# Kernel optimization log

Hardware: AMD Instinct MI355X
Metric: run time of the kernel (lower is better)

## Reference

```python
import jax, jax.numpy as jnp
import numpy as np

N = 4096
IN, HID, OUT = 512, 512, 512
EMB, MHID = 64, 128
GRID_SIZE, SPLINE_ORDER = 5, 3
D_B = GRID_SIZE + SPLINE_ORDER + 1      # 9
SPLINE_DIM = GRID_SIZE + SPLINE_ORDER   # 8


def make_grid():
    h = (1.0 - (-1.0)) / GRID_SIZE
    return jnp.arange(-SPLINE_ORDER, GRID_SIZE + SPLINE_ORDER + 1, dtype=jnp.float32) * h - 1.0


def b_splines(x, grid):
    # x: (N, in) -> (N, in, SPLINE_DIM); Cox-de Boor recursion, epsilon-stabilized
    xg = x[..., None]
    bases = ((xg >= grid[:-1]) & (xg < grid[1:])).astype(x.dtype)
    eps = 1e-08
    for k in range(1, SPLINE_ORDER + 1):
        dp = grid[k:-1] - grid[:-(k + 1)]
        dn = grid[k + 1:] - grid[1:-k]
        bases = (xg - grid[:-(k + 1)]) / (dp + eps) * bases[..., :-1] \
              + (grid[k + 1:] - xg) / (dn + eps) * bases[..., 1:]
    return bases


def _xavier(k, shape):
    fan_out, fan_in = shape
    std = (2.0 / (fan_in + fan_out)) ** 0.5
    return std * jax.random.normal(k, shape, jnp.float32)


def setup_inputs() -> dict:
    key = jax.random.key(0)
    ks = jax.random.split(key, 7)
    x = 2.0 * jax.random.uniform(ks[0], (N, IN), jnp.float32) - 1.0
    inp = {"x": x}
    dims = [(IN, HID), (HID, OUT)]
    for i, (fi, fo) in enumerate(dims):
        kk = jax.random.split(ks[i + 1], 3)
        inp[f"emb{i}"] = _xavier(kk[0], (fi * fo, EMB))   # layout: (out, in) flattened, out outer
        inp[f"w1_{i}"] = _xavier(kk[1], (MHID, EMB))
        inp[f"b1_{i}"] = jnp.zeros((MHID,), jnp.float32)
        inp[f"w2_{i}"] = _xavier(kk[2], (D_B, MHID))
        inp[f"b2_{i}"] = jnp.zeros((D_B,), jnp.float32)
    return inp


def _kan_layer(h, emb, w1, b1, w2, b2, in_f, out_f, grid):
    basis = b_splines(h, grid)                              # (N, in, SPLINE_DIM)
    w = (emb @ w1.T + b1) @ w2.T + b2                       # (out*in, D_B)
    w = w.reshape(out_f, in_f, D_B)
    w_spline = w[..., :SPLINE_DIM]                          # (out, in, SPLINE_DIM)
    w_base = w[..., SPLINE_DIM]                             # (out, in)  == weights[:, :, -1]
    out = jnp.einsum('nis,ois->no', basis, w_spline)
    out = out + jnp.einsum('ni,oi->no', jax.nn.silu(h), w_base)
    return out


def reference(x, emb0, w1_0, b1_0, w2_0, b2_0, emb1, w1_1, b1_1, w2_1, b2_1):
    grid = make_grid()
    h = _kan_layer(x, emb0, w1_0, b1_0, w2_0, b2_0, IN, HID, grid)
    h = _kan_layer(h, emb1, w1_1, b1_1, w2_1, b2_1, HID, OUT, grid)
    return h
```

## Files before the change

kernel.cpp:

```cpp
#include <hip/hip_runtime.h>
#include <cstdint>
#include <cstddef>

typedef unsigned short u16;
typedef unsigned int   u32;

typedef __bf16 bf16x8 __attribute__((ext_vector_type(8)));
typedef float  f32x4  __attribute__((ext_vector_type(4)));

#define NROWS 4096
#define INF   512
#define OUTF  512
#define EMB   64
#define MHID  128
#define DB    9
#define KDIM  (INF * DB)
#define MN    (NROWS * OUTF)

__device__ __forceinline__ u16 f2bf(float f) {
    union { float f; u32 ui; } v; v.f = f;
    u32 u = v.ui;
    u += 0x7fffu + ((u >> 16) & 1u);
    return (u16)(u >> 16);
}
__device__ __forceinline__ float gridv(int t) { return (float)(t - 3) * 0.4f - 1.0f; }

__global__ __launch_bounds__(256) void meff_kernel(
    const float* __restrict__ w1_0, const float* __restrict__ b1_0,
    const float* __restrict__ w2_0, const float* __restrict__ b2_0,
    const float* __restrict__ w1_1, const float* __restrict__ b1_1,
    const float* __restrict__ w2_1, const float* __restrict__ b2_1,
    float* __restrict__ Mc)
{
    int tid  = threadIdx.x;
    int lane = tid & 63;
    int wid  = blockIdx.x * 4 + (tid >> 6);
    if (wid >= 1170) return;
    int layer = wid / 585;
    int o     = wid % 585;
    const float* w1 = layer ? w1_1 : w1_0;
    const float* b1 = layer ? b1_1 : b1_0;
    const float* w2 = layer ? w2_1 : w2_0;
    const float* b2 = layer ? b2_1 : b2_0;

    float p;
    int d;
    if (o < 576) {
        int j = o / 9; d = o % 9;
        p = w1[lane * EMB + j]        * w2[d * MHID + lane]
          + w1[(lane + 64) * EMB + j] * w2[d * MHID + lane + 64];
    } else {
        d = o - 576;
        p = b1[lane] * w2[d * MHID + lane] + b1[lane + 64] * w2[d * MHID + lane + 64];
    }
#pragma unroll
    for (int off = 32; off >= 1; off >>= 1)
        p += __shfl_xor(p, off, 64);
    if (lane == 0) {
        if (o >= 576) p += b2[d];
        Mc[layer * 1024 + o] = p;
    }
}

__global__ __launch_bounds__(256) void genw_kernel(
    const float* __restrict__ emb0, const float* __restrict__ emb1,
    const float* __restrict__ Mc,
    u16* __restrict__ Bw0, u16* __restrict__ Bw1)
{
    __shared__ __align__(16) float tile[256 * 65];
    __shared__ float Ms[64 * 12];
    __shared__ float Cs[9];

    int layer = blockIdx.y;
    const float* emb = layer ? emb1 : emb0;
    u16* Bw = layer ? Bw1 : Bw0;
    const float* mc = Mc + layer * 1024;

    int tid = threadIdx.x;
    for (int idx = tid; idx < 585; idx += 256) {
        float v = mc[idx];
        if (idx < 576) Ms[(idx / 9) * 12 + (idx % 9)] = v;
        else Cs[idx - 576] = v;
    }

    size_t rowbase = (size_t)blockIdx.x * 256;
    const float4* g4 = (const float4*)(emb + rowbase * EMB);
#pragma unroll
    for (int it = 0; it < 16; ++it) {
        int f = it * 256 + tid;
        float4 v = g4[f];
        int row = f >> 4, c4 = (f & 15) * 4;
        float* t = &tile[row * 65 + c4];
        t[0] = v.x; t[1] = v.y; t[2] = v.z; t[3] = v.w;
    }
    __syncthreads();

    float acc[9];
#pragma unroll
    for (int d = 0; d < 9; ++d) acc[d] = Cs[d];

    const float* myrow = &tile[tid * 65];
#pragma unroll
    for (int jj = 0; jj < 16; ++jj) {
        float v0 = myrow[jj * 4 + 0];
        float v1 = myrow[jj * 4 + 1];
        float v2 = myrow[jj * 4 + 2];
        float v3 = myrow[jj * 4 + 3];
        const float* m0 = &Ms[(jj * 4 + 0) * 12];
        const float* m1 = &Ms[(jj * 4 + 1) * 12];
        const float* m2 = &Ms[(jj * 4 + 2) * 12];
        const float* m3 = &Ms[(jj * 4 + 3) * 12];
#pragma unroll
        for (int d = 0; d < 9; ++d)
            acc[d] += v0 * m0[d] + v1 * m1[d] + v2 * m2[d] + v3 * m3[d];
    }

    __syncthreads();
    u16* ob = (u16*)tile;
#pragma unroll
    for (int d = 0; d < 9; ++d) ob[tid * 9 + d] = f2bf(acc[d]);
    __syncthreads();

    const uint4* src = (const uint4*)ob;
    uint4* dst = (uint4*)(Bw + rowbase * 9);
    for (int s = tid; s < 288; s += 256) dst[s] = src[s];
}

__global__ __launch_bounds__(256) void phi_kernel(const float* __restrict__ xin,
                                                  const float* __restrict__ part,
                                                  int S,
                                                  u16* __restrict__ phi)
{
    __shared__ __align__(16) u16 lbuf[256 * 9];
    int tid = threadIdx.x;
    int idx = blockIdx.x * 256 + tid;

    float xv;
    if (part) {
        xv = 0.f;
        for (int z = 0; z < S; ++z) xv += part[(size_t)z * MN + idx];
    } else {
        xv = xin[idx];
    }

    float b[11];
#pragma unroll
    for (int t = 0; t < 11; ++t)
        b[t] = (xv >= gridv(t) && xv < gridv(t + 1)) ? 1.0f : 0.0f;
#pragma unroll
    for (int k = 1; k <= 3; ++k) {
#pragma unroll
        for (int t = 0; t + k < 11; ++t) {
            float dp = (gridv(t + k) - gridv(t)) + 1e-8f;
            float dn = (gridv(t + k + 1) - gridv(t + 1)) + 1e-8f;
            b[t] = (xv - gridv(t)) / dp * b[t] + (gridv(t + k + 1) - xv) / dn * b[t + 1];
        }
    }
    float sil = xv / (1.0f + expf(-xv));

#pragma unroll
    for (int d = 0; d < 8; ++d) lbuf[tid * 9 + d] = f2bf(b[d]);
    lbuf[tid * 9 + 8] = f2bf(sil);
    __syncthreads();

    const uint4* src = (const uint4*)lbuf;
    uint4* dst = (uint4*)(phi + (size_t)blockIdx.x * 256 * 9);
    for (int s = tid; s < 288; s += 256) dst[s] = src[s];
}

#define GLOAD16(gp, lp) __builtin_amdgcn_global_load_lds(                         \
    (const __attribute__((address_space(1))) u32*)(gp),                           \
    (__attribute__((address_space(3))) u32*)(lp), 16, 0, 0)

__global__ __launch_bounds__(256, 4) void gemm_kernel(const __bf16* __restrict__ A,
                                                      const __bf16* __restrict__ B,
                                                      float* __restrict__ Cpart,
                                                      int N, int K, int ksz)
{
    __shared__ __align__(16) __bf16 As[128 * 64];
    __shared__ __align__(16) __bf16 Bs[128 * 64];

    int tid  = threadIdx.x;
    int lane = tid & 63;
    int wv   = tid >> 6;
    int wm   = wv >> 1, wn = wv & 1;
    int brow = blockIdx.x * 128;
    int bcol = blockIdx.y * 128;
    int z    = blockIdx.z;
    int kbeg = z * ksz, kend = kbeg + ksz;

    f32x4 acc[4][4];
#pragma unroll
    for (int r = 0; r < 4; ++r)
#pragma unroll
        for (int c = 0; c < 4; ++c)
#pragma unroll
            for (int g = 0; g < 4; ++g) acc[r][c][g] = 0.0f;

    int quad = lane >> 4;
    int l16  = lane & 15;

    for (int k0 = kbeg; k0 < kend; k0 += 64) {
#pragma unroll
        for (int q = 0; q < 4; ++q) {
            int chunk = q * 256 + wv * 64 + lane;
            int row   = chunk >> 3;
            int slot  = chunk & 7;
            int col   = ((slot ^ (row & 7)) << 3);
            const __bf16* ga = A + (size_t)(brow + row) * K + (k0 + col);
            const __bf16* gb = B + (size_t)(bcol + row) * K + (k0 + col);
            GLOAD16(ga, &As[(q * 256 + wv * 64) * 8]);
            GLOAD16(gb, &Bs[(q * 256 + wv * 64) * 8]);
        }
        __syncthreads();

#pragma unroll
        for (int ks = 0; ks < 2; ++ks) {
            bf16x8 af[4], bfr[4];
#pragma unroll
            for (int r = 0; r < 4; ++r) {
                int arow = wm * 64 + r * 16 + l16;
                af[r] = *(const bf16x8*)&As[arow * 64 + (((ks * 4 + quad) ^ (arow & 7)) << 3)];
                int brw = wn * 64 + r * 16 + l16;
                bfr[r] = *(const bf16x8*)&Bs[brw * 64 + (((ks * 4 + quad) ^ (brw & 7)) << 3)];
            }
#pragma unroll
            for (int r = 0; r < 4; ++r)
#pragma unroll
                for (int c = 0; c < 4; ++c)
                    acc[r][c] = __builtin_amdgcn_mfma_f32_16x16x32_bf16(af[r], bfr[c], acc[r][c], 0, 0, 0);
        }
        __syncthreads();
    }

    float* Cz = Cpart + (size_t)z * MN;
#pragma unroll
    for (int r = 0; r < 4; ++r)
#pragma unroll
        for (int c = 0; c < 4; ++c)
#pragma unroll
            for (int g = 0; g < 4; ++g) {
                int grow = brow + wm * 64 + r * 16 + quad * 4 + g;
                int gcol = bcol + wn * 64 + c * 16 + l16;
                Cz[(size_t)grow * N + gcol] = acc[r][c][g];
            }
}

__global__ __launch_bounds__(256) void reduce_kernel(const float* __restrict__ part,
                                                     int S, float* __restrict__ out)
{
    int i = blockIdx.x * 256 + threadIdx.x;
    const float4* p4 = (const float4*)part;
    float4 s = p4[i];
    for (int z = 1; z < S; ++z) {
        float4 v = p4[(size_t)z * (MN / 4) + i];
        s.x += v.x; s.y += v.y; s.z += v.z; s.w += v.w;
    }
    ((float4*)out)[i] = s;
}

extern "C" void kernel_launch(void* const* d_in, const int* in_sizes, int n_in,
                              void* d_out, int out_size, void* d_ws, size_t ws_size,
                              hipStream_t stream)
{
    const float* x    = (const float*)d_in[0];
    const float* emb0 = (const float*)d_in[1];
    const float* w1_0 = (const float*)d_in[2];
    const float* b1_0 = (const float*)d_in[3];
    const float* w2_0 = (const float*)d_in[4];
    const float* b2_0 = (const float*)d_in[5];
    const float* emb1 = (const float*)d_in[6];
    const float* w1_1 = (const float*)d_in[7];
    const float* b1_1 = (const float*)d_in[8];
    const float* w2_1 = (const float*)d_in[9];
    const float* b2_1 = (const float*)d_in[10];

    char* ws = (char*)d_ws;
    const size_t PHI_OFF  = 0;
    const size_t BW0_OFF  = 37748736;
    const size_t BW1_OFF  = BW0_OFF + 4718592;
    const size_t MC_OFF   = BW1_OFF + 4718592;
    const size_t PART_OFF = MC_OFF + 8192;

    int S = 1;
    if (ws_size >= PART_OFF + 4ull * 8388608) S = 4;
    else if (ws_size >= PART_OFF + 2ull * 8388608) S = 2;
    int ksz = KDIM / S;

    u16*   phi  = (u16*)(ws + PHI_OFF);
    u16*   Bw0  = (u16*)(ws + BW0_OFF);
    u16*   Bw1  = (u16*)(ws + BW1_OFF);
    float* Mc   = (float*)(ws + MC_OFF);
    float* part = (float*)(ws + PART_OFF);

    meff_kernel<<<293, 256, 0, stream>>>(w1_0, b1_0, w2_0, b2_0,
                                         w1_1, b1_1, w2_1, b2_1, Mc);
    genw_kernel<<<dim3(1024, 2), 256, 0, stream>>>(emb0, emb1, Mc, Bw0, Bw1);

    phi_kernel<<<8192, 256, 0, stream>>>(x, nullptr, 0, phi);
    gemm_kernel<<<dim3(32, 4, S), 256, 0, stream>>>((const __bf16*)phi, (const __bf16*)Bw0,
                                                    part, OUTF, KDIM, ksz);
    phi_kernel<<<8192, 256, 0, stream>>>(nullptr, part, S, phi);
    gemm_kernel<<<dim3(32, 4, S), 256, 0, stream>>>((const __bf16*)phi, (const __bf16*)Bw1,
                                                    part, OUTF, KDIM, ksz);
    reduce_kernel<<<2048, 256, 0, stream>>>(part, S, (float*)d_out);
}
```

Measured before the change: 323.3 us.

## Restructure genw to four rows per thread and allow deeper split-K

The weight-generation kernel now has each thread process four embedding rows, loading them directly from global memory as float4 instead of staging through a padded LDS tile. Each LDS read of the Ms coefficients is reused across four rows, and the grid shrinks to a quarter of the blocks. Separately, the split-K factor can now rise to 3, 6 or 8 when the workspace is large enough, which adds GEMM parallelism but also more partial-sum traffic in the reduce and phi passes. The strided direct global loads may coalesce less well than the old staged tile.

```diff
diff --git a/kernel.cpp b/kernel.cpp
--- a/kernel.cpp
+++ b/kernel.cpp
@@ -67,9 +67,9 @@
     const float* __restrict__ Mc,
     u16* __restrict__ Bw0, u16* __restrict__ Bw1)
 {
-    __shared__ __align__(16) float tile[256 * 65];
     __shared__ float Ms[64 * 12];
     __shared__ float Cs[9];
+    __shared__ __align__(16) u16 ob[1024 * 9];
 
     int layer = blockIdx.y;
     const float* emb = layer ? emb1 : emb0;
@@ -82,48 +82,46 @@
         if (idx < 576) Ms[(idx / 9) * 12 + (idx % 9)] = v;
         else Cs[idx - 576] = v;
     }
-
-    size_t rowbase = (size_t)blockIdx.x * 256;
+    __syncthreads();
+
+    size_t rowbase = (size_t)blockIdx.x * 1024;
+    float acc[4][9];
+#pragma unroll
+    for (int r = 0; r < 4; ++r)
+#pragma unroll
+        for (int d = 0; d < 9; ++d) acc[r][d] = Cs[d];
+
     const float4* g4 = (const float4*)(emb + rowbase * EMB);
 #pragma unroll
-    for (int it = 0; it < 16; ++it) {
-        int f = it * 256 + tid;
-        float4 v = g4[f];
-        int row = f >> 4, c4 = (f & 15) * 4;
-        float* t = &tile[row * 65 + c4];
-        t[0] = v.x; t[1] = v.y; t[2] = v.z; t[3] = v.w;
-    }
-    __syncthreads();
-
-    float acc[9];
-#pragma unroll
-    for (int d = 0; d < 9; ++d) acc[d] = Cs[d];
-
-    const float* myrow = &tile[tid * 65];
-#pragma unroll
     for (int jj = 0; jj < 16; ++jj) {
-        float v0 = myrow[jj * 4 + 0];
-        float v1 = myrow[jj * 4 + 1];
-        float v2 = myrow[jj * 4 + 2];
-        float v3 = myrow[jj * 4 + 3];
-        const float* m0 = &Ms[(jj * 4 + 0) * 12];
-        const float* m1 = &Ms[(jj * 4 + 1) * 12];
-        const float* m2 = &Ms[(jj * 4 + 2) * 12];
-        const float* m3 = &Ms[(jj * 4 + 3) * 12];
+        float vv[4][4];
+#pragma unroll
+        for (int r = 0; r < 4; ++r)
+            *(float4*)vv[r] = g4[(size_t)(r * 256 + tid) * 16 + jj];
+#pragma unroll
+        for (int t = 0; t < 4; ++t) {
+            const float* m = &Ms[(jj * 4 + t) * 12];
+#pragma unroll
+            for (int d = 0; d < 9; ++d) {
+                float mv = m[d];
+                acc[0][d] += vv[0][t] * mv;
+                acc[1][d] += vv[1][t] * mv;
+                acc[2][d] += vv[2][t] * mv;
+                acc[3][d] += vv[3][t] * mv;
+            }
+        }
+    }
+
+#pragma unroll
+    for (int r = 0; r < 4; ++r)
 #pragma unroll
         for (int d = 0; d < 9; ++d)
-            acc[d] += v0 * m0[d] + v1 * m1[d] + v2 * m2[d] + v3 * m3[d];
-    }
-
-    __syncthreads();
-    u16* ob = (u16*)tile;
-#pragma unroll
-    for (int d = 0; d < 9; ++d) ob[tid * 9 + d] = f2bf(acc[d]);
+            ob[(r * 256 + tid) * 9 + d] = f2bf(acc[r][d]);
     __syncthreads();
 
     const uint4* src = (const uint4*)ob;
     uint4* dst = (uint4*)(Bw + rowbase * 9);
-    for (int s = tid; s < 288; s += 256) dst[s] = src[s];
+    for (int s = tid; s < 1152; s += 256) dst[s] = src[s];
 }
 
 __global__ __launch_bounds__(256) void phi_kernel(const float* __restrict__ xin,
@@ -283,8 +281,12 @@
     const size_t PART_OFF = MC_OFF + 8192;
 
     int S = 1;
-    if (ws_size >= PART_OFF + 4ull * 8388608) S = 4;
-    else if (ws_size >= PART_OFF + 2ull * 8388608) S = 2;
+    const size_t SLAB = 8388608ull;
+    if      (ws_size >= PART_OFF + 8 * SLAB) S = 8;
+    else if (ws_size >= PART_OFF + 6 * SLAB) S = 6;
+    else if (ws_size >= PART_OFF + 4 * SLAB) S = 4;
+    else if (ws_size >= PART_OFF + 3 * SLAB) S = 3;
+    else if (ws_size >= PART_OFF + 2 * SLAB) S = 2;
     int ksz = KDIM / S;
 
     u16*   phi  = (u16*)(ws + PHI_OFF);
@@ -295,7 +297,7 @@
 
     meff_kernel<<<293, 256, 0, stream>>>(w1_0, b1_0, w2_0, b2_0,
                                          w1_1, b1_1, w2_1, b2_1, Mc);
-    genw_kernel<<<dim3(1024, 2), 256, 0, stream>>>(emb0, emb1, Mc, Bw0, Bw1);
+    genw_kernel<<<dim3(256, 2), 256, 0, stream>>>(emb0, emb1, Mc, Bw0, Bw1);
 
     phi_kernel<<<8192, 256, 0, stream>>>(x, nullptr, 0, phi);
     gemm_kernel<<<dim3(32, 4, S), 256, 0, stream>>>((const __bf16*)phi, (const __bf16*)Bw0,
```

New measurement: 388.1 us. 20.0% more time.
